# Kernel optimization log

Hardware: AMD Instinct MI355X
Metric: run time of the kernel (lower is better)

## Reference

```python
import jax, jax.numpy as jnp
import numpy as np
import math

D = 512; NA = 128; NC = 256; NB = 128; BATCH = 4; H = 8
EA, EC, EB = 4, 6, 4
KA, KC, KB = 2, 1, 2
F = 4 * D  # expert_ff_mult * embed_dim
N_TOTAL = NA + NC + NB


def setup_inputs() -> dict:
    key = jax.random.key(0)
    ks = jax.random.split(key, 16)
    s = 0.02
    def nrm(k, shape, scale=s):
        return jax.random.normal(k, shape, dtype=jnp.float32) * scale
    return {
        'tokens_A': jax.random.normal(ks[0], (BATCH, NA, D), dtype=jnp.float32),
        'tokens_B': jax.random.normal(ks[1], (BATCH, NB, D), dtype=jnp.float32),
        'tokens_C': jax.random.normal(ks[2], (BATCH, NC, D), dtype=jnp.float32),
        'ln1_g': jnp.ones((3, D), jnp.float32), 'ln1_b': jnp.zeros((3, D), jnp.float32),
        'ln2_g': jnp.ones((3, D), jnp.float32), 'ln2_b': jnp.zeros((3, D), jnp.float32),
        'Wqkv': nrm(ks[3], (3 * D, D)), 'bqkv': jnp.zeros((3 * D,), jnp.float32),
        'Wo': nrm(ks[4], (D, D)), 'bo': jnp.zeros((D,), jnp.float32),
        'Wr_A': nrm(ks[5], (D, EA)), 'br_A': jnp.zeros((EA,), jnp.float32),
        'W1_A': nrm(ks[6], (EA, D, F)), 'b1_A': jnp.zeros((EA, F), jnp.float32),
        'W2_A': nrm(ks[7], (EA, F, D)), 'b2_A': jnp.zeros((EA, D), jnp.float32),
        'Wr_C': nrm(ks[8], (D, EC)), 'br_C': jnp.zeros((EC,), jnp.float32),
        'W1_C': nrm(ks[9], (EC, D, F)), 'b1_C': jnp.zeros((EC, F), jnp.float32),
        'W2_C': nrm(ks[10], (EC, F, D)), 'b2_C': jnp.zeros((EC, D), jnp.float32),
        'Wr_B': nrm(ks[11], (D, EB)), 'br_B': jnp.zeros((EB,), jnp.float32),
        'W1_B': nrm(ks[12], (EB, D, F)), 'b1_B': jnp.zeros((EB, F), jnp.float32),
        'W2_B': nrm(ks[13], (EB, F, D)), 'b2_B': jnp.zeros((EB, D), jnp.float32),
    }


def _ln(x, g, b, eps=1e-5):
    m = jnp.mean(x, axis=-1, keepdims=True)
    v = jnp.var(x, axis=-1, keepdims=True)
    return (x - m) * jax.lax.rsqrt(v + eps) * g + b


def _directed_mask_bias():
    # segments: 0=A, 1=C, 2=B in [A|C|B] order; query may attend upstream groups only
    seg = jnp.concatenate([jnp.zeros(NA), jnp.ones(NC), 2.0 * jnp.ones(NB)])
    allowed = seg[None, :] <= seg[:, None]  # (N, N)
    return jnp.where(allowed, 0.0, -1e9).astype(jnp.float32)


def _mha(x, Wqkv, bqkv, Wo, bo, mask_bias):
    B, N, _ = x.shape
    qkv = x @ Wqkv.T + bqkv  # (B, N, 3D)
    q, k, v = jnp.split(qkv, 3, axis=-1)
    hd = D // H
    def heads(t):
        return t.reshape(B, N, H, hd).transpose(0, 2, 1, 3)  # (B, H, N, hd)
    q, k, v = heads(q), heads(k), heads(v)
    scores = jnp.einsum('bhqd,bhkd->bhqk', q, k) / math.sqrt(hd) + mask_bias[None, None]
    attn = jax.nn.softmax(scores, axis=-1)
    o = jnp.einsum('bhqk,bhkd->bhqd', attn, v).transpose(0, 2, 1, 3).reshape(B, N, D)
    return o @ Wo.T + bo


def _moe(x, Wr, br, W1, b1, W2, b2, k):
    # top-k routed expert FFN: softmax gates -> top-k renormalized -> dense combine
    probs = jax.nn.softmax(x @ Wr + br, axis=-1)  # (B, N, E)
    vals, idx = jax.lax.top_k(probs, k)
    vals = vals / jnp.sum(vals, axis=-1, keepdims=True)
    E = Wr.shape[1]
    gate = jnp.sum(jax.nn.one_hot(idx, E, dtype=x.dtype) * vals[..., None], axis=-2)  # (B, N, E)
    h = jax.nn.gelu(jnp.einsum('bnd,edf->benf', x, W1) + b1[None, :, None, :])
    y = jnp.einsum('benf,efd->bend', h, W2) + b2[None, :, None, :]
    return jnp.einsum('bne,bend->bnd', gate, y)


def reference(tokens_A, tokens_B, tokens_C, ln1_g, ln1_b, ln2_g, ln2_b,
              Wqkv, bqkv, Wo, bo,
              Wr_A, br_A, W1_A, b1_A, W2_A, b2_A,
              Wr_C, br_C, W1_C, b1_C, W2_C, b2_C,
              Wr_B, br_B, W1_B, b1_B, W2_B, b2_B):
    # 1-2. group-local pre-attention LN, concat [A | C | B]
    x = jnp.concatenate([
        _ln(tokens_A, ln1_g[0], ln1_b[0]),
        _ln(tokens_C, ln1_g[1], ln1_b[1]),
        _ln(tokens_B, ln1_g[2], ln1_b[2]),
    ], axis=1)
    # 3-4. shared directed self-attention + per-group residual
    attn = _mha(x, Wqkv, bqkv, Wo, bo, _directed_mask_bias())
    tA = tokens_A + attn[:, :NA]
    tC = tokens_C + attn[:, NA:NA + NC]
    tB = tokens_B + attn[:, NA + NC:]
    # 5. group-local pre-expert LN
    nA = _ln(tA, ln2_g[0], ln2_b[0])
    nC = _ln(tC, ln2_g[1], ln2_b[1])
    nB = _ln(tB, ln2_g[2], ln2_b[2])
    # 6-9. route A and C first, then B; residual add per group
    tA = tA + _moe(nA, Wr_A, br_A, W1_A, b1_A, W2_A, b2_A, KA)
    tC = tC + _moe(nC, Wr_C, br_C, W1_C, b1_C, W2_C, b2_C, KC)
    tB = tB + _moe(nB, Wr_B, br_B, W1_B, b1_B, W2_B, b2_B, KB)
    return jnp.concatenate([tA, tC, tB], axis=1)  # (B, NA+NC+NB, D)
```

## Files before the change

kernel.cpp:

```cpp
#include <hip/hip_runtime.h>
#include <hip/hip_bf16.h>
#include <cstdint>

#define DEV __device__ __forceinline__

using f32x4  = __attribute__((ext_vector_type(4))) float;
using bf16x8 = __attribute__((ext_vector_type(8))) __bf16;

static constexpr int D_    = 512;
static constexpr int ROWS  = 2048;
static constexpr int F_    = 2048;
static constexpr int NEXP  = 14;
static constexpr int NENT  = 3072;

DEV unsigned short f2bf(float f) {
  unsigned int u = __builtin_bit_cast(unsigned int, f);
  unsigned int r = u + 0x7FFFu + ((u >> 16) & 1u);
  return (unsigned short)(r >> 16);
}
DEV unsigned int pack2(float a, float b) {
  return (unsigned int)f2bf(a) | ((unsigned int)f2bf(b) << 16);
}
DEV float gelu_tanh(float x) {
  float x3 = x * x * x;
  return 0.5f * x * (1.0f + tanhf(0.7978845608028654f * (x + 0.044715f * x3)));
}

struct Shared128 { unsigned short As[128][72]; unsigned short Bs[64][72]; };

DEV void gemm128(const unsigned short* arow, const float* B, int ldb, int bcol0, int K,
                 f32x4 (&acc)[2][4], Shared128& sh)
{
  const int tid = threadIdx.x;
  const int lane = tid & 63, w = tid >> 6;
  const int ai = tid >> 1, ah = tid & 1;
  const int bj = tid >> 2, bq = tid & 3;
  for (int k0 = 0; k0 < K; k0 += 64) {
    __syncthreads();
    {
      const uint4* src = reinterpret_cast<const uint4*>(arow + k0 + ah * 32);
      uint4 v0 = src[0], v1 = src[1], v2 = src[2], v3 = src[3];
      uint4* dst = reinterpret_cast<uint4*>(&sh.As[ai][ah * 32]);
      dst[0] = v0; dst[1] = v1; dst[2] = v2; dst[3] = v3;
    }
    {
      const float4* src = reinterpret_cast<const float4*>(B + (size_t)(bcol0 + bj) * ldb + k0 + bq * 16);
      unsigned int pk[8];
      #pragma unroll
      for (int u = 0; u < 4; ++u) {
        float4 f = src[u];
        pk[u * 2]     = pack2(f.x, f.y);
        pk[u * 2 + 1] = pack2(f.z, f.w);
      }
      uint4* dst = reinterpret_cast<uint4*>(&sh.Bs[bj][bq * 16]);
      dst[0] = make_uint4(pk[0], pk[1], pk[2], pk[3]);
      dst[1] = make_uint4(pk[4], pk[5], pk[6], pk[7]);
    }
    __syncthreads();
    #pragma unroll
    for (int ks = 0; ks < 2; ++ks) {
      bf16x8 a[2], b[4];
      #pragma unroll
      for (int mi = 0; mi < 2; ++mi)
        a[mi] = *reinterpret_cast<const bf16x8*>(&sh.As[w * 32 + mi * 16 + (lane & 15)][ks * 32 + (lane >> 4) * 8]);
      #pragma unroll
      for (int ni = 0; ni < 4; ++ni)
        b[ni] = *reinterpret_cast<const bf16x8*>(&sh.Bs[ni * 16 + (lane & 15)][ks * 32 + (lane >> 4) * 8]);
      #pragma unroll
      for (int mi = 0; mi < 2; ++mi)
        #pragma unroll
        for (int ni = 0; ni < 4; ++ni)
          acc[mi][ni] = __builtin_amdgcn_mfma_f32_16x16x32_bf16(a[mi], b[ni], acc[mi][ni], 0, 0, 0);
    }
  }
}

struct Shared64x128 { unsigned short As[64][72]; unsigned short Bs[128][72]; };

DEV void gemm64x128(const unsigned short* arow, const unsigned short* B, int ldb, int bcol0, int K,
                    f32x4 (&acc)[8], Shared64x128& sh)
{
  const int tid = threadIdx.x;
  const int lane = tid & 63, w = tid >> 6;
  const int ar = tid >> 2, aq = tid & 3;
  const int br = tid >> 1, bh = tid & 1;
  for (int k0 = 0; k0 < K; k0 += 64) {
    __syncthreads();
    {
      const uint4* srcA = reinterpret_cast<const uint4*>(arow + k0 + aq * 16);
      uint4 a0 = srcA[0], a1 = srcA[1];
      uint4* dstA = reinterpret_cast<uint4*>(&sh.As[ar][aq * 16]);
      dstA[0] = a0; dstA[1] = a1;
      const uint4* srcB = reinterpret_cast<const uint4*>(B + (size_t)(bcol0 + br) * ldb + k0 + bh * 32);
      uint4 b0 = srcB[0], b1 = srcB[1], b2 = srcB[2], b3 = srcB[3];
      uint4* dstB = reinterpret_cast<uint4*>(&sh.Bs[br][bh * 32]);
      dstB[0] = b0; dstB[1] = b1; dstB[2] = b2; dstB[3] = b3;
    }
    __syncthreads();
    #pragma unroll
    for (int ks = 0; ks < 2; ++ks) {
      bf16x8 a = *reinterpret_cast<const bf16x8*>(&sh.As[w * 16 + (lane & 15)][ks * 32 + (lane >> 4) * 8]);
      #pragma unroll
      for (int ni = 0; ni < 8; ++ni) {
        bf16x8 b = *reinterpret_cast<const bf16x8*>(&sh.Bs[ni * 16 + (lane & 15)][ks * 32 + (lane >> 4) * 8]);
        acc[ni] = __builtin_amdgcn_mfma_f32_16x16x32_bf16(a, b, acc[ni], 0, 0, 0);
      }
    }
  }
}

__global__ __launch_bounds__(256) void k_ln(
    const float* tA, const float* tC, const float* tB,
    const float* g3, const float* b3, unsigned short* out)
{
  int r = blockIdx.x;
  int b = r >> 9, n = r & 511;
  int grp = n < 128 ? 0 : (n < 384 ? 1 : 2);
  const float* src = grp == 0 ? tA + (size_t)(b * 128 + n) * D_
                   : grp == 1 ? tC + (size_t)(b * 256 + n - 128) * D_
                              : tB + (size_t)(b * 128 + n - 384) * D_;
  int tid = threadIdx.x, lane = tid & 63, w = tid >> 6;
  float2 v = *reinterpret_cast<const float2*>(src + tid * 2);
  float s = v.x + v.y;
  float ss = v.x * v.x + v.y * v.y;
  #pragma unroll
  for (int off = 1; off < 64; off <<= 1) { s += __shfl_xor(s, off); ss += __shfl_xor(ss, off); }
  __shared__ float red[8];
  if (lane == 0) { red[w] = s; red[4 + w] = ss; }
  __syncthreads();
  float S  = red[0] + red[1] + red[2] + red[3];
  float SS = red[4] + red[5] + red[6] + red[7];
  float mean = S * (1.0f / 512.0f);
  float var  = SS * (1.0f / 512.0f) - mean * mean;
  float inv  = rsqrtf(var + 1e-5f);
  const float* gam = g3 + grp * D_;
  const float* bet = b3 + grp * D_;
  int d0 = tid * 2;
  out[(size_t)r * D_ + d0]     = f2bf((v.x - mean) * inv * gam[d0]     + bet[d0]);
  out[(size_t)r * D_ + d0 + 1] = f2bf((v.y - mean) * inv * gam[d0 + 1] + bet[d0 + 1]);
}

__global__ __launch_bounds__(256) void k_qkv(const unsigned short* x, const float* Wqkv, const float* bqkv,
                                             unsigned short* Qg, unsigned short* Kg, unsigned short* Vg)
{
  __shared__ Shared128 sh;
  int bn = blockIdx.x, bm = blockIdx.y, batch = blockIdx.z;
  int tid = threadIdx.x, lane = tid & 63, w = tid >> 6;
  const unsigned short* arow = x + (size_t)(batch * 512 + bm * 128 + (tid >> 1)) * D_;
  f32x4 acc[2][4] = {};
  gemm128(arow, Wqkv, 512, bn * 64, 512, acc, sh);
  #pragma unroll
  for (int mi = 0; mi < 2; ++mi)
  #pragma unroll
  for (int ni = 0; ni < 4; ++ni)
  #pragma unroll
  for (int j = 0; j < 4; ++j) {
    int n = bm * 128 + w * 32 + mi * 16 + ((lane >> 4) << 2) + j;
    int col = bn * 64 + ni * 16 + (lane & 15);
    float val = acc[mi][ni][j] + bqkv[col];
    int part = col >> 9;
    int o = col & 511, h = o >> 6, d = o & 63;
    unsigned short* dst = part == 0 ? Qg : (part == 1 ? Kg : Vg);
    dst[(size_t)((batch * 8 + h) * 512 + n) * 64 + d] = f2bf(val);
  }
}

__global__ __launch_bounds__(256) void k_attn(const unsigned short* Qg, const unsigned short* Kg,
                                              const unsigned short* Vg, unsigned short* attn)
{
  __shared__ unsigned short Qs[64][72], Ks[64][72], VT[64][72], Ps[64][72];
  int qt = blockIdx.x, h = blockIdx.y, b = blockIdx.z;
  int tid = threadIdx.x, lane = tid & 63, w = tid >> 6;
  const unsigned short* Qb  = Qg + (size_t)((b * 8 + h) * 512) * 64;
  const unsigned short* Kbp = Kg + (size_t)((b * 8 + h) * 512) * 64;
  const unsigned short* Vbp = Vg + (size_t)((b * 8 + h) * 512) * 64;
  int i4 = tid >> 2, q4 = tid & 3;
  {
    const uint4* src = reinterpret_cast<const uint4*>(Qb + (size_t)(qt * 64 + i4) * 64 + q4 * 16);
    uint4 v0 = src[0], v1 = src[1];
    uint4* dst = reinterpret_cast<uint4*>(&Qs[i4][q4 * 16]);
    dst[0] = v0; dst[1] = v1;
  }
  int nkt = qt < 2 ? 2 : (qt < 6 ? 6 : 8);
  float mrun[4] = { -1e30f, -1e30f, -1e30f, -1e30f };
  float lrun[4] = {};
  f32x4 o[4] = {};
  for (int kt = 0; kt < nkt; ++kt) {
    __syncthreads();
    {
      const uint4* src = reinterpret_cast<const uint4*>(Kbp + (size_t)(kt * 64 + i4) * 64 + q4 * 16);
      uint4 v0 = src[0], v1 = src[1];
      uint4* dst = reinterpret_cast<uint4*>(&Ks[i4][q4 * 16]);
      dst[0] = v0; dst[1] = v1;
      union { uint4 u[2]; unsigned short s[16]; } vv;
      const uint4* vsrc = reinterpret_cast<const uint4*>(Vbp + (size_t)(kt * 64 + i4) * 64 + q4 * 16);
      vv.u[0] = vsrc[0]; vv.u[1] = vsrc[1];
      #pragma unroll
      for (int jj = 0; jj < 16; ++jj) VT[q4 * 16 + jj][i4] = vv.s[jj];
    }
    __syncthreads();
    f32x4 s[4] = {};
    #pragma unroll
    for (int ks = 0; ks < 2; ++ks) {
      bf16x8 aq = *reinterpret_cast<const bf16x8*>(&Qs[w * 16 + (lane & 15)][ks * 32 + (lane >> 4) * 8]);
      #pragma unroll
      for (int cc = 0; cc < 4; ++cc) {
        bf16x8 bk = *reinterpret_cast<const bf16x8*>(&Ks[cc * 16 + (lane & 15)][ks * 32 + (lane >> 4) * 8]);
        s[cc] = __builtin_amdgcn_mfma_f32_16x16x32_bf16(aq, bk, s[cc], 0, 0, 0);
      }
    }
    #pragma unroll
    for (int rr = 0; rr < 4; ++rr) {
      float s0 = s[0][rr] * 0.125f, s1 = s[1][rr] * 0.125f;
      float s2 = s[2][rr] * 0.125f, s3 = s[3][rr] * 0.125f;
      float mx = fmaxf(fmaxf(s0, s1), fmaxf(s2, s3));
      #pragma unroll
      for (int off = 1; off < 16; off <<= 1) mx = fmaxf(mx, __shfl_xor(mx, off));
      float mn = fmaxf(mrun[rr], mx);
      float al = expf(mrun[rr] - mn);
      mrun[rr] = mn;
      float p0 = expf(s0 - mn), p1 = expf(s1 - mn), p2 = expf(s2 - mn), p3 = expf(s3 - mn);
      float ps = p0 + p1 + p2 + p3;
      #pragma unroll
      for (int off = 1; off < 16; off <<= 1) ps += __shfl_xor(ps, off);
      lrun[rr] = lrun[rr] * al + ps;
      #pragma unroll
      for (int n4 = 0; n4 < 4; ++n4) o[n4][rr] *= al;
      int prow = w * 16 + ((lane >> 4) << 2) + rr;
      Ps[prow][0 * 16 + (lane & 15)] = f2bf(p0);
      Ps[prow][1 * 16 + (lane & 15)] = f2bf(p1);
      Ps[prow][2 * 16 + (lane & 15)] = f2bf(p2);
      Ps[prow][3 * 16 + (lane & 15)] = f2bf(p3);
    }
    __syncthreads();
    #pragma unroll
    for (int ks = 0; ks < 2; ++ks) {
      bf16x8 ap = *reinterpret_cast<const bf16x8*>(&Ps[w * 16 + (lane & 15)][ks * 32 + (lane >> 4) * 8]);
      #pragma unroll
      for (int n4 = 0; n4 < 4; ++n4) {
        bf16x8 bv = *reinterpret_cast<const bf16x8*>(&VT[n4 * 16 + (lane & 15)][ks * 32 + (lane >> 4) * 8]);
        o[n4] = __builtin_amdgcn_mfma_f32_16x16x32_bf16(ap, bv, o[n4], 0, 0, 0);
      }
    }
  }
  #pragma unroll
  for (int n4 = 0; n4 < 4; ++n4)
  #pragma unroll
  for (int rr = 0; rr < 4; ++rr) {
    int qrow = qt * 64 + w * 16 + ((lane >> 4) << 2) + rr;
    int col = h * 64 + n4 * 16 + (lane & 15);
    float val = o[n4][rr] / lrun[rr];
    attn[(size_t)(b * 512 + qrow) * 512 + col] = f2bf(val);
  }
}

__global__ __launch_bounds__(256) void k_wo(const unsigned short* attn, const float* Wo, const float* bo,
                                            const float* tokA, const float* tokC, const float* tokB,
                                            float* out)
{
  __shared__ Shared128 sh;
  int bn = blockIdx.x, bm = blockIdx.y;
  int tid = threadIdx.x, lane = tid & 63, w = tid >> 6;
  const unsigned short* arow = attn + (size_t)(bm * 128 + (tid >> 1)) * D_;
  f32x4 acc[2][4] = {};
  gemm128(arow, Wo, 512, bn * 64, 512, acc, sh);
  #pragma unroll
  for (int mi = 0; mi < 2; ++mi)
  #pragma unroll
  for (int ni = 0; ni < 4; ++ni)
  #pragma unroll
  for (int j = 0; j < 4; ++j) {
    int row = bm * 128 + w * 32 + mi * 16 + ((lane >> 4) << 2) + j;
    int col = bn * 64 + ni * 16 + (lane & 15);
    float val = acc[mi][ni][j] + bo[col];
    int b = row >> 9, n = row & 511;
    float res;
    if (n < 128)      res = tokA[(size_t)(b * 128 + n) * D_ + col];
    else if (n < 384) res = tokC[(size_t)(b * 256 + n - 128) * D_ + col];
    else              res = tokB[(size_t)(b * 128 + n - 384) * D_ + col];
    out[(size_t)row * D_ + col] = res + val;
  }
}

template<int E, int TOPK, int EGBASE, int SEG0, int NSEG>
__global__ __launch_bounds__(256) void k_router(const float* t,
    const float* ln2g, const float* ln2b, const float* Wr, const float* br,
    int* cnt, int* tokexp, float* tokgate, unsigned short* nrm)
{
  constexpr int GRP = EGBASE == 0 ? 0 : (EGBASE == 4 ? 1 : 2);
  constexpr int BPB = NSEG / 4;
  int w = threadIdx.x >> 6, lane = threadIdx.x & 63;
  int b = blockIdx.x / BPB, i = blockIdx.x % BPB;
  int r = b * 512 + SEG0 + i * 4 + w;
  const float* tr = t + (size_t)r * D_;
  float xv[8];
  float s = 0.0f, ss = 0.0f;
  #pragma unroll
  for (int it = 0; it < 8; ++it) {
    float v = tr[it * 64 + lane];
    xv[it] = v; s += v; ss += v * v;
  }
  #pragma unroll
  for (int off = 1; off < 64; off <<= 1) { s += __shfl_xor(s, off); ss += __shfl_xor(ss, off); }
  float mean = s * (1.0f / 512.0f);
  float var  = ss * (1.0f / 512.0f) - mean * mean;
  float inv  = rsqrtf(var + 1e-5f);
  const float* gam = ln2g + GRP * D_;
  const float* bet = ln2b + GRP * D_;
  float acc[E] = {};
  #pragma unroll
  for (int it = 0; it < 8; ++it) {
    int d = it * 64 + lane;
    float nv = (xv[it] - mean) * inv * gam[d] + bet[d];
    nrm[(size_t)r * D_ + d] = f2bf(nv);
    #pragma unroll
    for (int e = 0; e < E; ++e) acc[e] += nv * Wr[d * E + e];
  }
  #pragma unroll
  for (int e = 0; e < E; ++e)
    #pragma unroll
    for (int off = 1; off < 64; off <<= 1) acc[e] += __shfl_xor(acc[e], off);
  if (lane == 0) {
    float p[E];
    float mx = -1e30f;
    #pragma unroll
    for (int e = 0; e < E; ++e) { p[e] = acc[e] + br[e]; mx = fmaxf(mx, p[e]); }
    float sum = 0.0f;
    #pragma unroll
    for (int e = 0; e < E; ++e) { p[e] = expf(p[e] - mx); sum += p[e]; }
    #pragma unroll
    for (int e = 0; e < E; ++e) p[e] /= sum;
    int i1 = 0; float v1 = p[0];
    #pragma unroll
    for (int e = 1; e < E; ++e) if (p[e] > v1) { v1 = p[e]; i1 = e; }
    if (TOPK == 1) {
      tokexp[r * 2]     = EGBASE + i1; tokgate[r * 2]     = 1.0f;
      tokexp[r * 2 + 1] = -1;          tokgate[r * 2 + 1] = 0.0f;
      atomicAdd(&cnt[EGBASE + i1], 1);
    } else {
      int i2 = -1; float v2 = -1e30f;
      #pragma unroll
      for (int e = 0; e < E; ++e) if (e != i1 && p[e] > v2) { v2 = p[e]; i2 = e; }
      float tot = v1 + v2;
      tokexp[r * 2]     = EGBASE + i1; tokgate[r * 2]     = v1 / tot;
      tokexp[r * 2 + 1] = EGBASE + i2; tokgate[r * 2 + 1] = v2 / tot;
      atomicAdd(&cnt[EGBASE + i1], 1);
      atomicAdd(&cnt[EGBASE + i2], 1);
    }
  }
}

__global__ void k_scan(const int* cnt, int* base) {
  if (threadIdx.x == 0) {
    int acc = 0;
    for (int e = 0; e < NEXP; ++e) { base[e] = acc; acc += cnt[e]; }
  }
}
__global__ __launch_bounds__(256) void k_scatter(const int* tokexp, const float* tokgate,
                                                 const int* base, int* cursor, int* list, float* gate)
{
  int r = blockIdx.x * 256 + threadIdx.x;
  #pragma unroll
  for (int j = 0; j < 2; ++j) {
    int e = tokexp[r * 2 + j];
    if (e >= 0) {
      int s = atomicAdd(&cursor[e], 1);
      list[base[e] + s] = r;
      gate[base[e] + s] = tokgate[r * 2 + j];
    }
  }
}

__global__ __launch_bounds__(256) void k_trAll(
    const float* w1A, const float* w1C, const float* w1B,
    const float* w2A, const float* w2C, const float* w2B,
    unsigned short* W1T, unsigned short* W2T)
{
  int bx = blockIdx.x, z = blockIdx.y;
  const float* src;
  unsigned short* dst;
  int ldS, ldD, R0, C0;
  if (z < 14) {
    int e = z;
    src = e < 4 ? w1A + (size_t)e * D_ * F_ : e < 10 ? w1C + (size_t)(e - 4) * D_ * F_ : w1B + (size_t)(e - 10) * D_ * F_;
    dst = W1T + (size_t)e * F_ * D_;
    ldS = F_; ldD = D_;
    R0 = (bx & 3) * 128;
    C0 = (bx >> 2) * 32;
  } else {
    int e = z - 14;
    src = e < 4 ? w2A + (size_t)e * F_ * D_ : e < 10 ? w2C + (size_t)(e - 4) * F_ * D_ : w2B + (size_t)(e - 10) * F_ * D_;
    dst = W2T + (size_t)e * D_ * F_;
    ldS = D_; ldD = F_;
    R0 = (bx & 15) * 128;
    C0 = (bx >> 4) * 32;
  }
  __shared__ float tile[128][33];
  int t = threadIdx.x;
  {
    int r = t >> 1, h = t & 1;
    const float4* sp = reinterpret_cast<const float4*>(src + (size_t)(R0 + r) * ldS + C0 + h * 16);
    #pragma unroll
    for (int u = 0; u < 4; ++u) {
      float4 v = sp[u];
      tile[r][h * 16 + u * 4 + 0] = v.x; tile[r][h * 16 + u * 4 + 1] = v.y;
      tile[r][h * 16 + u * 4 + 2] = v.z; tile[r][h * 16 + u * 4 + 3] = v.w;
    }
  }
  __syncthreads();
  {
    int c = t >> 3, g = t & 7;
    unsigned int pk[8];
    #pragma unroll
    for (int i = 0; i < 8; ++i) {
      float fa = tile[g * 16 + 2 * i][c];
      float fb = tile[g * 16 + 2 * i + 1][c];
      pk[i] = pack2(fa, fb);
    }
    uint4* dp = reinterpret_cast<uint4*>(dst + (size_t)(C0 + c) * ldD + R0 + g * 16);
    dp[0] = make_uint4(pk[0], pk[1], pk[2], pk[3]);
    dp[1] = make_uint4(pk[4], pk[5], pk[6], pk[7]);
  }
}

__global__ __launch_bounds__(256) void k_moe1(const unsigned short* nrm, const unsigned short* W1T,
    const float* b1A, const float* b1C, const float* b1B,
    const int* cnt, const int* ebase, const int* list, unsigned short* H)
{
  int ft = blockIdx.x, tt = blockIdx.y, e = blockIdx.z;
  int c = cnt[e];
  if (tt * 64 >= c) return;
  __shared__ Shared64x128 sh;
  const float* b1 = e < 4 ? b1A + (size_t)e * F_ : e < 10 ? b1C + (size_t)(e - 4) * F_ : b1B + (size_t)(e - 10) * F_;
  const unsigned short* Wt = W1T + (size_t)e * F_ * D_;
  int base = ebase[e];
  int tid = threadIdx.x, lane = tid & 63, w = tid >> 6;
  int ig = tt * 64 + (tid >> 2);
  int tok = list[base + (ig < c ? ig : c - 1)];
  const unsigned short* arow = nrm + (size_t)tok * D_;
  f32x4 acc[8] = {};
  gemm64x128(arow, Wt, 512, ft * 128, 512, acc, sh);
  #pragma unroll
  for (int ni = 0; ni < 8; ++ni)
  #pragma unroll
  for (int j = 0; j < 4; ++j) {
    int rl = w * 16 + ((lane >> 4) << 2) + j;
    int sg = tt * 64 + rl;
    if (sg < c) {
      int col = ft * 128 + ni * 16 + (lane & 15);
      float val = acc[ni][j] + b1[col];
      H[(size_t)(base + sg) * F_ + col] = f2bf(gelu_tanh(val));
    }
  }
}

__global__ __launch_bounds__(256) void k_moe2(const unsigned short* H, const unsigned short* W2T,
    const float* b2A, const float* b2C, const float* b2B,
    const int* cnt, const int* ebase, const int* list, const float* gate, float* out)
{
  int dt = blockIdx.x, tt = blockIdx.y >> 2, kc = blockIdx.y & 3, e = blockIdx.z;
  int c = cnt[e];
  if (tt * 64 >= c) return;
  __shared__ Shared64x128 sh;
  const float* b2 = e < 4 ? b2A + (size_t)e * D_ : e < 10 ? b2C + (size_t)(e - 4) * D_ : b2B + (size_t)(e - 10) * D_;
  const unsigned short* Wt = W2T + (size_t)e * D_ * F_ + kc * 512;
  int base = ebase[e];
  int tid = threadIdx.x, lane = tid & 63, w = tid >> 6;
  int ig = tt * 64 + (tid >> 2);
  const unsigned short* arow = H + (size_t)(base + (ig < c ? ig : c - 1)) * F_ + kc * 512;
  f32x4 acc[8] = {};
  gemm64x128(arow, Wt, F_, dt * 128, 512, acc, sh);
  #pragma unroll
  for (int ni = 0; ni < 8; ++ni)
  #pragma unroll
  for (int j = 0; j < 4; ++j) {
    int rl = w * 16 + ((lane >> 4) << 2) + j;
    int sg = tt * 64 + rl;
    if (sg < c) {
      int col = dt * 128 + ni * 16 + (lane & 15);
      float val = acc[ni][j] + (kc == 0 ? b2[col] : 0.0f);
      int tok = list[base + sg];
      atomicAdd(&out[(size_t)tok * D_ + col], gate[base + sg] * val);
    }
  }
}

extern "C" void kernel_launch(void* const* d_in, const int* in_sizes, int n_in,
                              void* d_out, int out_size, void* d_ws, size_t ws_size,
                              hipStream_t stream)
{
  const float* tokA = (const float*)d_in[0];
  const float* tokB = (const float*)d_in[1];
  const float* tokC = (const float*)d_in[2];
  const float* ln1g = (const float*)d_in[3];
  const float* ln1b = (const float*)d_in[4];
  const float* ln2g = (const float*)d_in[5];
  const float* ln2b = (const float*)d_in[6];
  const float* Wqkv = (const float*)d_in[7];
  const float* bqkv = (const float*)d_in[8];
  const float* Wo   = (const float*)d_in[9];
  const float* bo   = (const float*)d_in[10];
  const float* WrA  = (const float*)d_in[11];
  const float* brA  = (const float*)d_in[12];
  const float* W1A  = (const float*)d_in[13];
  const float* b1A  = (const float*)d_in[14];
  const float* W2A  = (const float*)d_in[15];
  const float* b2A  = (const float*)d_in[16];
  const float* WrC  = (const float*)d_in[17];
  const float* brC  = (const float*)d_in[18];
  const float* W1C  = (const float*)d_in[19];
  const float* b1C  = (const float*)d_in[20];
  const float* W2C  = (const float*)d_in[21];
  const float* b2C  = (const float*)d_in[22];
  const float* WrB  = (const float*)d_in[23];
  const float* brB  = (const float*)d_in[24];
  const float* W1B  = (const float*)d_in[25];
  const float* b1B  = (const float*)d_in[26];
  const float* W2B  = (const float*)d_in[27];
  const float* b2B  = (const float*)d_in[28];
  float* out = (float*)d_out;

  char* ws = (char*)d_ws;
  const size_t MB = 1024 * 1024;
  const size_t WSTRIDE = (size_t)NEXP * F_ * D_ * 2;
  unsigned short* xb   = (unsigned short*)(ws);
  unsigned short* nrm  = xb;
  unsigned short* Qg   = (unsigned short*)(ws + 2 * MB);
  unsigned short* Kg   = (unsigned short*)(ws + 4 * MB);
  unsigned short* Vg   = (unsigned short*)(ws + 6 * MB);
  unsigned short* attn = (unsigned short*)(ws + 8 * MB);
  unsigned short* W1T  = (unsigned short*)(ws + 16 * MB);
  unsigned short* W2T  = (unsigned short*)(ws + 16 * MB + WSTRIDE);
  unsigned short* H    = (unsigned short*)(ws + 16 * MB + 2 * WSTRIDE);
  char* small = ws + 16 * MB + 2 * WSTRIDE + (size_t)NENT * F_ * 2;
  int*   cnt     = (int*)(small);
  int*   cursor  = (int*)(small + 64);
  int*   ebase   = (int*)(small + 128);
  int*   tokexp  = (int*)(small + 256);
  float* tokgate = (float*)(small + 256 + ROWS * 2 * 4);
  int*   list    = (int*)(small + 256 + ROWS * 4 * 4);
  float* gate    = (float*)(small + 256 + ROWS * 4 * 4 + NENT * 4);

  hipMemsetAsync(cnt, 0, 192, stream);
  k_ln<<<ROWS, 256, 0, stream>>>(tokA, tokC, tokB, ln1g, ln1b, xb);
  k_qkv<<<dim3(24, 4, 4), 256, 0, stream>>>(xb, Wqkv, bqkv, Qg, Kg, Vg);
  k_attn<<<dim3(8, 8, 4), 256, 0, stream>>>(Qg, Kg, Vg, attn);
  k_wo<<<dim3(8, 16), 256, 0, stream>>>(attn, Wo, bo, tokA, tokC, tokB, out);
  k_router<4, 2, 0,  0,   128><<<128, 256, 0, stream>>>(out, ln2g, ln2b, WrA, brA, cnt, tokexp, tokgate, nrm);
  k_router<6, 1, 4,  128, 256><<<256, 256, 0, stream>>>(out, ln2g, ln2b, WrC, brC, cnt, tokexp, tokgate, nrm);
  k_router<4, 2, 10, 384, 128><<<128, 256, 0, stream>>>(out, ln2g, ln2b, WrB, brB, cnt, tokexp, tokgate, nrm);
  k_scan<<<1, 64, 0, stream>>>(cnt, ebase);
  k_scatter<<<8, 256, 0, stream>>>(tokexp, tokgate, ebase, cursor, list, gate);
  k_trAll<<<dim3(256, 28), 256, 0, stream>>>(W1A, W1C, W1B, W2A, W2C, W2B, W1T, W2T);
  k_moe1<<<dim3(16, 16, 14), 256, 0, stream>>>(nrm, W1T, b1A, b1C, b1B, cnt, ebase, list, H);
  k_moe2<<<dim3(4, 64, 14), 256, 0, stream>>>(H, W2T, b2A, b2C, b2B, cnt, ebase, list, gate, out);
}
```

Measured before the change: 236.9 us.

## Merge router launches, drop scan kernel, shrink attention blocks, retile weight transpose

Folds the three templated router launches into one kernel that picks its group per row. The separate prefix-scan kernel is removed, and each consumer now recomputes expert base offsets from the counts. Attention switches to single-wavefront blocks of 16 queries, which removes the block barriers and gives four times as many blocks, but each block reloads K/V tiles itself. The weight transpose uses square 64x64 tiles on a 3D grid. Together these cut launch count and sync overhead, at the cost of redundant K/V loads and runtime branching in the router.

```diff
diff --git a/kernel.cpp b/kernel.cpp
--- a/kernel.cpp
+++ b/kernel.cpp
@@ -24,6 +24,11 @@
 DEV float gelu_tanh(float x) {
   float x3 = x * x * x;
   return 0.5f * x * (1.0f + tanhf(0.7978845608028654f * (x + 0.044715f * x3)));
+}
+DEV int prefix_base(const int* cnt, int e) {
+  int base = 0;
+  for (int i = 0; i < e; ++i) base += cnt[i];
+  return base;
 }
 
 struct Shared128 { unsigned short As[128][72]; unsigned short Bs[64][72]; };
@@ -165,44 +170,46 @@
   }
 }
 
-__global__ __launch_bounds__(256) void k_attn(const unsigned short* Qg, const unsigned short* Kg,
-                                              const unsigned short* Vg, unsigned short* attn)
-{
-  __shared__ unsigned short Qs[64][72], Ks[64][72], VT[64][72], Ps[64][72];
-  int qt = blockIdx.x, h = blockIdx.y, b = blockIdx.z;
-  int tid = threadIdx.x, lane = tid & 63, w = tid >> 6;
+__global__ __launch_bounds__(64) void k_attn(const unsigned short* Qg, const unsigned short* Kg,
+                                             const unsigned short* Vg, unsigned short* attn)
+{
+  __shared__ unsigned short Qs[16][72], Ks[64][72], VT[64][72], Ps[16][72];
+  int qt16 = blockIdx.x, h = blockIdx.y, b = blockIdx.z;
+  int lane = threadIdx.x;
   const unsigned short* Qb  = Qg + (size_t)((b * 8 + h) * 512) * 64;
   const unsigned short* Kbp = Kg + (size_t)((b * 8 + h) * 512) * 64;
   const unsigned short* Vbp = Vg + (size_t)((b * 8 + h) * 512) * 64;
-  int i4 = tid >> 2, q4 = tid & 3;
+  int q0 = qt16 * 16;
   {
-    const uint4* src = reinterpret_cast<const uint4*>(Qb + (size_t)(qt * 64 + i4) * 64 + q4 * 16);
-    uint4 v0 = src[0], v1 = src[1];
-    uint4* dst = reinterpret_cast<uint4*>(&Qs[i4][q4 * 16]);
-    dst[0] = v0; dst[1] = v1;
-  }
-  int nkt = qt < 2 ? 2 : (qt < 6 ? 6 : 8);
+    int row = lane >> 2, q4 = lane & 3;
+    const uint4* src = reinterpret_cast<const uint4*>(Qb + (size_t)(q0 + row) * 64 + q4 * 16);
+    uint4* dst = reinterpret_cast<uint4*>(&Qs[row][q4 * 16]);
+    dst[0] = src[0]; dst[1] = src[1];
+  }
+  int nkt = qt16 < 8 ? 2 : (qt16 < 24 ? 6 : 8);
   float mrun[4] = { -1e30f, -1e30f, -1e30f, -1e30f };
   float lrun[4] = {};
   f32x4 o[4] = {};
   for (int kt = 0; kt < nkt; ++kt) {
-    __syncthreads();
-    {
-      const uint4* src = reinterpret_cast<const uint4*>(Kbp + (size_t)(kt * 64 + i4) * 64 + q4 * 16);
-      uint4 v0 = src[0], v1 = src[1];
-      uint4* dst = reinterpret_cast<uint4*>(&Ks[i4][q4 * 16]);
-      dst[0] = v0; dst[1] = v1;
-      union { uint4 u[2]; unsigned short s[16]; } vv;
-      const uint4* vsrc = reinterpret_cast<const uint4*>(Vbp + (size_t)(kt * 64 + i4) * 64 + q4 * 16);
-      vv.u[0] = vsrc[0]; vv.u[1] = vsrc[1];
-      #pragma unroll
-      for (int jj = 0; jj < 16; ++jj) VT[q4 * 16 + jj][i4] = vv.s[jj];
-    }
-    __syncthreads();
+    #pragma unroll
+    for (int it = 0; it < 4; ++it) {
+      int row = it * 16 + (lane >> 2), q4 = lane & 3;
+      const uint4* ksrc = reinterpret_cast<const uint4*>(Kbp + (size_t)(kt * 64 + row) * 64 + q4 * 16);
+      uint4* kdst = reinterpret_cast<uint4*>(&Ks[row][q4 * 16]);
+      kdst[0] = ksrc[0]; kdst[1] = ksrc[1];
+      union { uint4 u; unsigned short s[8]; } vv0, vv1;
+      const uint4* vsrc = reinterpret_cast<const uint4*>(Vbp + (size_t)(kt * 64 + row) * 64 + q4 * 16);
+      vv0.u = vsrc[0]; vv1.u = vsrc[1];
+      #pragma unroll
+      for (int jj = 0; jj < 8; ++jj) {
+        VT[q4 * 16 + jj][row]     = vv0.s[jj];
+        VT[q4 * 16 + 8 + jj][row] = vv1.s[jj];
+      }
+    }
     f32x4 s[4] = {};
     #pragma unroll
     for (int ks = 0; ks < 2; ++ks) {
-      bf16x8 aq = *reinterpret_cast<const bf16x8*>(&Qs[w * 16 + (lane & 15)][ks * 32 + (lane >> 4) * 8]);
+      bf16x8 aq = *reinterpret_cast<const bf16x8*>(&Qs[lane & 15][ks * 32 + (lane >> 4) * 8]);
       #pragma unroll
       for (int cc = 0; cc < 4; ++cc) {
         bf16x8 bk = *reinterpret_cast<const bf16x8*>(&Ks[cc * 16 + (lane & 15)][ks * 32 + (lane >> 4) * 8]);
@@ -226,16 +233,15 @@
       lrun[rr] = lrun[rr] * al + ps;
       #pragma unroll
       for (int n4 = 0; n4 < 4; ++n4) o[n4][rr] *= al;
-      int prow = w * 16 + ((lane >> 4) << 2) + rr;
+      int prow = ((lane >> 4) << 2) + rr;
       Ps[prow][0 * 16 + (lane & 15)] = f2bf(p0);
       Ps[prow][1 * 16 + (lane & 15)] = f2bf(p1);
       Ps[prow][2 * 16 + (lane & 15)] = f2bf(p2);
       Ps[prow][3 * 16 + (lane & 15)] = f2bf(p3);
     }
-    __syncthreads();
     #pragma unroll
     for (int ks = 0; ks < 2; ++ks) {
-      bf16x8 ap = *reinterpret_cast<const bf16x8*>(&Ps[w * 16 + (lane & 15)][ks * 32 + (lane >> 4) * 8]);
+      bf16x8 ap = *reinterpret_cast<const bf16x8*>(&Ps[lane & 15][ks * 32 + (lane >> 4) * 8]);
       #pragma unroll
       for (int n4 = 0; n4 < 4; ++n4) {
         bf16x8 bv = *reinterpret_cast<const bf16x8*>(&VT[n4 * 16 + (lane & 15)][ks * 32 + (lane >> 4) * 8]);
@@ -247,7 +253,7 @@
   for (int n4 = 0; n4 < 4; ++n4)
   #pragma unroll
   for (int rr = 0; rr < 4; ++rr) {
-    int qrow = qt * 64 + w * 16 + ((lane >> 4) << 2) + rr;
+    int qrow = q0 + ((lane >> 4) << 2) + rr;
     int col = h * 64 + n4 * 16 + (lane & 15);
     float val = o[n4][rr] / lrun[rr];
     attn[(size_t)(b * 512 + qrow) * 512 + col] = f2bf(val);
@@ -282,16 +288,21 @@
   }
 }
 
-template<int E, int TOPK, int EGBASE, int SEG0, int NSEG>
 __global__ __launch_bounds__(256) void k_router(const float* t,
-    const float* ln2g, const float* ln2b, const float* Wr, const float* br,
+    const float* ln2g, const float* ln2b,
+    const float* WrA, const float* brA, const float* WrC, const float* brC,
+    const float* WrB, const float* brB,
     int* cnt, int* tokexp, float* tokgate, unsigned short* nrm)
 {
-  constexpr int GRP = EGBASE == 0 ? 0 : (EGBASE == 4 ? 1 : 2);
-  constexpr int BPB = NSEG / 4;
   int w = threadIdx.x >> 6, lane = threadIdx.x & 63;
-  int b = blockIdx.x / BPB, i = blockIdx.x % BPB;
-  int r = b * 512 + SEG0 + i * 4 + w;
+  int r = blockIdx.x * 4 + w;
+  int n = r & 511;
+  int grp = n < 128 ? 0 : (n < 384 ? 1 : 2);
+  int E = grp == 1 ? 6 : 4;
+  int topk = grp == 1 ? 1 : 2;
+  int egbase = grp == 0 ? 0 : (grp == 1 ? 4 : 10);
+  const float* Wr = grp == 0 ? WrA : (grp == 1 ? WrC : WrB);
+  const float* br = grp == 0 ? brA : (grp == 1 ? brC : brB);
   const float* tr = t + (size_t)r * D_;
   float xv[8];
   float s = 0.0f, ss = 0.0f;
@@ -305,68 +316,63 @@
   float mean = s * (1.0f / 512.0f);
   float var  = ss * (1.0f / 512.0f) - mean * mean;
   float inv  = rsqrtf(var + 1e-5f);
-  const float* gam = ln2g + GRP * D_;
-  const float* bet = ln2b + GRP * D_;
-  float acc[E] = {};
+  const float* gam = ln2g + grp * D_;
+  const float* bet = ln2b + grp * D_;
+  float acc[6] = {};
   #pragma unroll
   for (int it = 0; it < 8; ++it) {
     int d = it * 64 + lane;
     float nv = (xv[it] - mean) * inv * gam[d] + bet[d];
     nrm[(size_t)r * D_ + d] = f2bf(nv);
     #pragma unroll
-    for (int e = 0; e < E; ++e) acc[e] += nv * Wr[d * E + e];
-  }
-  #pragma unroll
-  for (int e = 0; e < E; ++e)
+    for (int e = 0; e < 6; ++e) if (e < E) acc[e] += nv * Wr[d * E + e];
+  }
+  #pragma unroll
+  for (int e = 0; e < 6; ++e)
     #pragma unroll
     for (int off = 1; off < 64; off <<= 1) acc[e] += __shfl_xor(acc[e], off);
   if (lane == 0) {
-    float p[E];
+    float p[6];
     float mx = -1e30f;
     #pragma unroll
-    for (int e = 0; e < E; ++e) { p[e] = acc[e] + br[e]; mx = fmaxf(mx, p[e]); }
+    for (int e = 0; e < 6; ++e) if (e < E) { p[e] = acc[e] + br[e]; mx = fmaxf(mx, p[e]); }
     float sum = 0.0f;
     #pragma unroll
-    for (int e = 0; e < E; ++e) { p[e] = expf(p[e] - mx); sum += p[e]; }
-    #pragma unroll
-    for (int e = 0; e < E; ++e) p[e] /= sum;
+    for (int e = 0; e < 6; ++e) if (e < E) { p[e] = expf(p[e] - mx); sum += p[e]; }
+    #pragma unroll
+    for (int e = 0; e < 6; ++e) if (e < E) p[e] /= sum;
     int i1 = 0; float v1 = p[0];
     #pragma unroll
-    for (int e = 1; e < E; ++e) if (p[e] > v1) { v1 = p[e]; i1 = e; }
-    if (TOPK == 1) {
-      tokexp[r * 2]     = EGBASE + i1; tokgate[r * 2]     = 1.0f;
+    for (int e = 1; e < 6; ++e) if (e < E && p[e] > v1) { v1 = p[e]; i1 = e; }
+    if (topk == 1) {
+      tokexp[r * 2]     = egbase + i1; tokgate[r * 2]     = 1.0f;
       tokexp[r * 2 + 1] = -1;          tokgate[r * 2 + 1] = 0.0f;
-      atomicAdd(&cnt[EGBASE + i1], 1);
+      atomicAdd(&cnt[egbase + i1], 1);
     } else {
       int i2 = -1; float v2 = -1e30f;
       #pragma unroll
-      for (int e = 0; e < E; ++e) if (e != i1 && p[e] > v2) { v2 = p[e]; i2 = e; }
+      for (int e = 0; e < 6; ++e) if (e < E && e != i1 && p[e] > v2) { v2 = p[e]; i2 = e; }
       float tot = v1 + v2;
-      tokexp[r * 2]     = EGBASE + i1; tokgate[r * 2]     = v1 / tot;
-      tokexp[r * 2 + 1] = EGBASE + i2; tokgate[r * 2 + 1] = v2 / tot;
-      atomicAdd(&cnt[EGBASE + i1], 1);
-      atomicAdd(&cnt[EGBASE + i2], 1);
-    }
-  }
-}
-
-__global__ void k_scan(const int* cnt, int* base) {
-  if (threadIdx.x == 0) {
-    int acc = 0;
-    for (int e = 0; e < NEXP; ++e) { base[e] = acc; acc += cnt[e]; }
-  }
-}
+      tokexp[r * 2]     = egbase + i1; tokgate[r * 2]     = v1 / tot;
+      tokexp[r * 2 + 1] = egbase + i2; tokgate[r * 2 + 1] = v2 / tot;
+      atomicAdd(&cnt[egbase + i1], 1);
+      atomicAdd(&cnt[egbase + i2], 1);
+    }
+  }
+}
+
 __global__ __launch_bounds__(256) void k_scatter(const int* tokexp, const float* tokgate,
-                                                 const int* base, int* cursor, int* list, float* gate)
+                                                 const int* cnt, int* cursor, int* list, float* gate)
 {
   int r = blockIdx.x * 256 + threadIdx.x;
   #pragma unroll
   for (int j = 0; j < 2; ++j) {
     int e = tokexp[r * 2 + j];
     if (e >= 0) {
+      int base = prefix_base(cnt, e);
       int s = atomicAdd(&cursor[e], 1);
-      list[base[e] + s] = r;
-      gate[base[e] + s] = tokgate[r * 2 + j];
+      list[base + s] = r;
+      gate[base + s] = tokgate[r * 2 + j];
     }
   }
 }
@@ -376,7 +382,7 @@
     const float* w2A, const float* w2C, const float* w2B,
     unsigned short* W1T, unsigned short* W2T)
 {
-  int bx = blockIdx.x, z = blockIdx.y;
+  int bx = blockIdx.x, by = blockIdx.y, z = blockIdx.z;
   const float* src;
   unsigned short* dst;
   int ldS, ldD, R0, C0;
@@ -385,47 +391,42 @@
     src = e < 4 ? w1A + (size_t)e * D_ * F_ : e < 10 ? w1C + (size_t)(e - 4) * D_ * F_ : w1B + (size_t)(e - 10) * D_ * F_;
     dst = W1T + (size_t)e * F_ * D_;
     ldS = F_; ldD = D_;
-    R0 = (bx & 3) * 128;
-    C0 = (bx >> 2) * 32;
+    R0 = by * 64;
+    C0 = bx * 64;
   } else {
     int e = z - 14;
     src = e < 4 ? w2A + (size_t)e * F_ * D_ : e < 10 ? w2C + (size_t)(e - 4) * F_ * D_ : w2B + (size_t)(e - 10) * F_ * D_;
     dst = W2T + (size_t)e * D_ * F_;
     ldS = D_; ldD = F_;
-    R0 = (bx & 15) * 128;
-    C0 = (bx >> 4) * 32;
-  }
-  __shared__ float tile[128][33];
-  int t = threadIdx.x;
-  {
-    int r = t >> 1, h = t & 1;
-    const float4* sp = reinterpret_cast<const float4*>(src + (size_t)(R0 + r) * ldS + C0 + h * 16);
-    #pragma unroll
-    for (int u = 0; u < 4; ++u) {
-      float4 v = sp[u];
-      tile[r][h * 16 + u * 4 + 0] = v.x; tile[r][h * 16 + u * 4 + 1] = v.y;
-      tile[r][h * 16 + u * 4 + 2] = v.z; tile[r][h * 16 + u * 4 + 3] = v.w;
-    }
+    R0 = bx * 64;
+    C0 = by * 64;
+  }
+  __shared__ float tile[64][65];
+  int t = threadIdx.x, r = t >> 2, q = t & 3;
+  const float4* sp = reinterpret_cast<const float4*>(src + (size_t)(R0 + r) * ldS + C0 + q * 16);
+  #pragma unroll
+  for (int u = 0; u < 4; ++u) {
+    float4 v = sp[u];
+    tile[r][q * 16 + u * 4 + 0] = v.x; tile[r][q * 16 + u * 4 + 1] = v.y;
+    tile[r][q * 16 + u * 4 + 2] = v.z; tile[r][q * 16 + u * 4 + 3] = v.w;
   }
   __syncthreads();
-  {
-    int c = t >> 3, g = t & 7;
-    unsigned int pk[8];
-    #pragma unroll
-    for (int i = 0; i < 8; ++i) {
-      float fa = tile[g * 16 + 2 * i][c];
-      float fb = tile[g * 16 + 2 * i + 1][c];
-      pk[i] = pack2(fa, fb);
-    }
-    uint4* dp = reinterpret_cast<uint4*>(dst + (size_t)(C0 + c) * ldD + R0 + g * 16);
-    dp[0] = make_uint4(pk[0], pk[1], pk[2], pk[3]);
-    dp[1] = make_uint4(pk[4], pk[5], pk[6], pk[7]);
-  }
+  int c = t >> 2;
+  unsigned int pk[8];
+  #pragma unroll
+  for (int i = 0; i < 8; ++i) {
+    float fa = tile[q * 16 + 2 * i][c];
+    float fb = tile[q * 16 + 2 * i + 1][c];
+    pk[i] = pack2(fa, fb);
+  }
+  uint4* dp = reinterpret_cast<uint4*>(dst + (size_t)(C0 + c) * ldD + R0 + q * 16);
+  dp[0] = make_uint4(pk[0], pk[1], pk[2], pk[3]);
+  dp[1] = make_uint4(pk[4], pk[5], pk[6], pk[7]);
 }
 
 __global__ __launch_bounds__(256) void k_moe1(const unsigned short* nrm, const unsigned short* W1T,
     const float* b1A, const float* b1C, const float* b1B,
-    const int* cnt, const int* ebase, const int* list, unsigned short* H)
+    const int* cnt, const int* list, unsigned short* H)
 {
   int ft = blockIdx.x, tt = blockIdx.y, e = blockIdx.z;
   int c = cnt[e];
@@ -433,7 +434,7 @@
   __shared__ Shared64x128 sh;
   const float* b1 = e < 4 ? b1A + (size_t)e * F_ : e < 10 ? b1C + (size_t)(e - 4) * F_ : b1B + (size_t)(e - 10) * F_;
   const unsigned short* Wt = W1T + (size_t)e * F_ * D_;
-  int base = ebase[e];
+  int base = prefix_base(cnt, e);
   int tid = threadIdx.x, lane = tid & 63, w = tid >> 6;
   int ig = tt * 64 + (tid >> 2);
   int tok = list[base + (ig < c ? ig : c - 1)];
@@ -456,7 +457,7 @@
 
 __global__ __launch_bounds__(256) void k_moe2(const unsigned short* H, const unsigned short* W2T,
     const float* b2A, const float* b2C, const float* b2B,
-    const int* cnt, const int* ebase, const int* list, const float* gate, float* out)
+    const int* cnt, const int* list, const float* gate, float* out)
 {
   int dt = blockIdx.x, tt = blockIdx.y >> 2, kc = blockIdx.y & 3, e = blockIdx.z;
   int c = cnt[e];
@@ -464,7 +465,7 @@
   __shared__ Shared64x128 sh;
   const float* b2 = e < 4 ? b2A + (size_t)e * D_ : e < 10 ? b2C + (size_t)(e - 4) * D_ : b2B + (size_t)(e - 10) * D_;
   const unsigned short* Wt = W2T + (size_t)e * D_ * F_ + kc * 512;
-  int base = ebase[e];
+  int base = prefix_base(cnt, e);
   int tid = threadIdx.x, lane = tid & 63, w = tid >> 6;
   int ig = tt * 64 + (tid >> 2);
   const unsigned short* arow = H + (size_t)(base + (ig < c ? ig : c - 1)) * F_ + kc * 512;
@@ -535,23 +536,20 @@
   char* small = ws + 16 * MB + 2 * WSTRIDE + (size_t)NENT * F_ * 2;
   int*   cnt     = (int*)(small);
   int*   cursor  = (int*)(small + 64);
-  int*   ebase   = (int*)(small + 128);
   int*   tokexp  = (int*)(small + 256);
   float* tokgate = (float*)(small + 256 + ROWS * 2 * 4);
   int*   list    = (int*)(small + 256 + ROWS * 4 * 4);
   float* gate    = (float*)(small + 256 + ROWS * 4 * 4 + NENT * 4);
 
-  hipMemsetAsync(cnt, 0, 192, stream);
+  hipMemsetAsync(cnt, 0, 128, stream);
   k_ln<<<ROWS, 256, 0, stream>>>(tokA, tokC, tokB, ln1g, ln1b, xb);
   k_qkv<<<dim3(24, 4, 4), 256, 0, stream>>>(xb, Wqkv, bqkv, Qg, Kg, Vg);
-  k_attn<<<dim3(8, 8, 4), 256, 0, stream>>>(Qg, Kg, Vg, attn);
+  k_attn<<<dim3(32, 8, 4), 64, 0, stream>>>(Qg, Kg, Vg, attn);
   k_wo<<<dim3(8, 16), 256, 0, stream>>>(attn, Wo, bo, tokA, tokC, tokB, out);
-  k_router<4, 2, 0,  0,   128><<<128, 256, 0, stream>>>(out, ln2g, ln2b, WrA, brA, cnt, tokexp, tokgate, nrm);
-  k_router<6, 1, 4,  128, 256><<<256, 256, 0, stream>>>(out, ln2g, ln2b, WrC, brC, cnt, tokexp, tokgate, nrm);
-  k_router<4, 2, 10, 384, 128><<<128, 256, 0, stream>>>(out, ln2g, ln2b, WrB, brB, cnt, tokexp, tokgate, nrm);
-  k_scan<<<1, 64, 0, stream>>>(cnt, ebase);
-  k_scatter<<<8, 256, 0, stream>>>(tokexp, tokgate, ebase, cursor, list, gate);
-  k_trAll<<<dim3(256, 28), 256, 0, stream>>>(W1A, W1C, W1B, W2A, W2C, W2B, W1T, W2T);
-  k_moe1<<<dim3(16, 16, 14), 256, 0, stream>>>(nrm, W1T, b1A, b1C, b1B, cnt, ebase, list, H);
-  k_moe2<<<dim3(4, 64, 14), 256, 0, stream>>>(H, W2T, b2A, b2C, b2B, cnt, ebase, list, gate, out);
-}
+  k_router<<<512, 256, 0, stream>>>(out, ln2g, ln2b, WrA, brA, WrC, brC, WrB, brB,
+                                    cnt, tokexp, tokgate, nrm);
+  k_scatter<<<8, 256, 0, stream>>>(tokexp, tokgate, cnt, cursor, list, gate);
+  k_trAll<<<dim3(32, 8, 28), 256, 0, stream>>>(W1A, W1C, W1B, W2A, W2C, W2B, W1T, W2T);
+  k_moe1<<<dim3(16, 16, 14), 256, 0, stream>>>(nrm, W1T, b1A, b1C, b1B, cnt, list, H);
+  k_moe2<<<dim3(4, 64, 14), 256, 0, stream>>>(H, W2T, b2A, b2C, b2B, cnt, list, gate, out);
+}
```

Measured after the change: 230.2 us. 1.03x faster.
